# Kernel tuning notes

Hardware: AMD Instinct MI355X
Metric: run time of the kernel (lower is better)

## Reference

```python
import jax, jax.numpy as jnp
import numpy as np

N, E, D_IN, D_HID, D_OUT, R, B = 50000, 600000, 128, 128, 128, 8, 4


def setup_inputs() -> dict:
    key = jax.random.key(0)
    ks = jax.random.split(key, 12)
    s = 0.05
    return {
        "x": jax.random.normal(ks[0], (N, D_IN), jnp.float32),
        "edge_index": jax.random.randint(ks[1], (2, E), 0, N, jnp.int32),
        "edge_type": jax.random.randint(ks[2], (E,), 0, R, jnp.int32),
        "basis1": jax.random.normal(ks[3], (B, D_IN, D_HID), jnp.float32) * s,
        "comp1": jax.random.normal(ks[4], (R, B), jnp.float32) * s,
        "root1": jax.random.normal(ks[5], (D_IN, D_HID), jnp.float32) * s,
        "bias1": jnp.zeros((D_HID,), jnp.float32),
        "basis2": jax.random.normal(ks[6], (B, D_HID, D_OUT), jnp.float32) * s,
        "comp2": jax.random.normal(ks[7], (R, B), jnp.float32) * s,
        "root2": jax.random.normal(ks[8], (D_HID, D_OUT), jnp.float32) * s,
        "bias2": jnp.zeros((D_OUT,), jnp.float32),
    }


def _rgcn_conv(x, src, dst, etype, basis, comp, root, bias):
    # PyG RGCNConv (basis decomposition, aggr='mean' per relation):
    # out_i = x_i @ root + bias + sum_r mean_{e: type=r, dst=i} (x_src_e @ W_r)
    # W_r linear => aggregate raw features per (node, relation), then transform.
    n = x.shape[0]
    r = comp.shape[0]
    W = jnp.einsum('rb,bio->rio', comp, basis)          # [R, in, out]
    seg = dst * r + etype                               # [E] composite key
    agg = jax.ops.segment_sum(x[src], seg, num_segments=n * r)        # [N*R, in]
    cnt = jax.ops.segment_sum(jnp.ones_like(seg, x.dtype), seg, num_segments=n * r)
    mean = (agg / jnp.maximum(cnt, 1.0)[:, None]).reshape(n, r, -1)   # [N, R, in]
    return jnp.einsum('nri,rio->no', mean, W) + x @ root + bias


def reference(x, edge_index, edge_type, basis1, comp1, root1, bias1,
              basis2, comp2, root2, bias2):
    src, dst = edge_index[0], edge_index[1]
    h = _rgcn_conv(x, src, dst, edge_type, basis1, comp1, root1, bias1)
    h = jax.nn.relu(h)
    # dropout p=0.2 is identity in eval mode
    out = _rgcn_conv(h, src, dst, edge_type, basis2, comp2, root2, bias2)
    return out
```

## Files before the change

### kernel.cpp

```cpp
#include <hip/hip_runtime.h>

#define NN 50000
#define NE 600000
#define DD 128
#define RR 8
#define NBASIS 4
#define NR (NN * RR)
#define KTOT 640
#define KZ 512
#define MPAD 50048
#define KMASK 0x0FFFFFFF

typedef float f32x4 __attribute__((ext_vector_type(4)));
typedef float f32x2 __attribute__((ext_vector_type(2)));
typedef short bf16x8 __attribute__((ext_vector_type(8)));
typedef unsigned int u32x4 __attribute__((ext_vector_type(4)));

static __device__ __forceinline__ unsigned short f2b(float f) {
  union { float f; unsigned u; } c; c.f = f;
  unsigned u = c.u + 0x7fffu + ((c.u >> 16) & 1u);
  return (unsigned short)(u >> 16);
}
static __device__ __forceinline__ unsigned pack2(float lo, float hi) {
  return (unsigned)f2b(lo) | ((unsigned)f2b(hi) << 16);
}
static __device__ __forceinline__ float b2f_lo(unsigned v) {
  union { unsigned u; float f; } c; c.u = v << 16; return c.f;
}
static __device__ __forceinline__ float b2f_hi(unsigned v) {
  union { unsigned u; float f; } c; c.u = v & 0xffff0000u; return c.f;
}
static __device__ __forceinline__ f32x2 sp2(float s) {
  f32x2 r; r.x = s; r.y = s; return r;
}

static __device__ __forceinline__ void fma_bf(f32x2* A0, f32x2* A1, f32x2* A2,
                                              f32x2* A3, u32x4 v, float4 c) {
  f32x2 e0, e1, e2, e3;
  e0.x = b2f_lo(v.x); e0.y = b2f_hi(v.x);
  e1.x = b2f_lo(v.y); e1.y = b2f_hi(v.y);
  e2.x = b2f_lo(v.z); e2.y = b2f_hi(v.z);
  e3.x = b2f_lo(v.w); e3.y = b2f_hi(v.w);
  f32x2 cx = sp2(c.x), cy = sp2(c.y), cz = sp2(c.z), cw = sp2(c.w);
  A0[0] += cx * e0; A0[1] += cx * e1; A0[2] += cx * e2; A0[3] += cx * e3;
  A1[0] += cy * e0; A1[1] += cy * e1; A1[2] += cy * e2; A1[3] += cy * e3;
  A2[0] += cz * e0; A2[1] += cz * e1; A2[2] += cz * e2; A2[3] += cz * e3;
  A3[0] += cw * e0; A3[1] += cw * e1; A3[2] += cw * e2; A3[3] += cw * e3;
}

static __device__ __forceinline__ void reduce_store(
    const f32x2* A0, const f32x2* A1, const f32x2* A2, const f32x2* A3,
    int g, int q, int node, u32x4* __restrict__ Ab4) {
  float a0[8] = {A0[0].x, A0[0].y, A0[1].x, A0[1].y,
                 A0[2].x, A0[2].y, A0[3].x, A0[3].y};
  float a1[8] = {A1[0].x, A1[0].y, A1[1].x, A1[1].y,
                 A1[2].x, A1[2].y, A1[3].x, A1[3].y};
  float a2[8] = {A2[0].x, A2[0].y, A2[1].x, A2[1].y,
                 A2[2].x, A2[2].y, A2[3].x, A2[3].y};
  float a3[8] = {A3[0].x, A3[0].y, A3[1].x, A3[1].y,
                 A3[2].x, A3[2].y, A3[3].x, A3[3].y};
#pragma unroll
  for (int j = 0; j < 8; ++j) {
    a0[j] += __shfl_xor(a0[j], 16); a0[j] += __shfl_xor(a0[j], 32);
    a1[j] += __shfl_xor(a1[j], 16); a1[j] += __shfl_xor(a1[j], 32);
    a2[j] += __shfl_xor(a2[j], 16); a2[j] += __shfl_xor(a2[j], 32);
    a3[j] += __shfl_xor(a3[j], 16); a3[j] += __shfl_xor(a3[j], 32);
  }
  u32x4 wv;
  if (g == 0) {
    wv.x = pack2(a0[0], a0[1]); wv.y = pack2(a0[2], a0[3]);
    wv.z = pack2(a0[4], a0[5]); wv.w = pack2(a0[6], a0[7]);
  } else if (g == 1) {
    wv.x = pack2(a1[0], a1[1]); wv.y = pack2(a1[2], a1[3]);
    wv.z = pack2(a1[4], a1[5]); wv.w = pack2(a1[6], a1[7]);
  } else if (g == 2) {
    wv.x = pack2(a2[0], a2[1]); wv.y = pack2(a2[2], a2[3]);
    wv.z = pack2(a2[4], a2[5]); wv.w = pack2(a2[6], a2[7]);
  } else {
    wv.x = pack2(a3[0], a3[1]); wv.y = pack2(a3[2], a3[3]);
    wv.z = pack2(a3[4], a3[5]); wv.w = pack2(a3[6], a3[7]);
  }
  __builtin_nontemporal_store(wv, Ab4 + (size_t)node * 64 + g * 16 + q);
}

#define PREP_XB 12500
#define PREP_BT 320
#define PREP_CNT 2344
#define PREP_TOTAL (PREP_XB + 2 * PREP_BT + PREP_CNT)

__global__ __launch_bounds__(256) void prep_kernel(
    const float* __restrict__ x, const float* __restrict__ basis1,
    const float* __restrict__ root1, const float* __restrict__ basis2,
    const float* __restrict__ root2, const int* __restrict__ dst,
    const int* __restrict__ et, unsigned* __restrict__ xb,
    unsigned short* __restrict__ BT1, unsigned short* __restrict__ BT2,
    int* __restrict__ cnt) {
  int bid = blockIdx.x;
  int t = threadIdx.x;
  if (bid < PREP_XB) {
    int i = bid * 256 + t;
    float2 v = ((const float2*)x)[i];
    xb[i] = pack2(v.x, v.y);
  } else if (bid < PREP_XB + PREP_BT) {
    int idx = (bid - PREP_XB) * 256 + t;
    int c = idx / KTOT, k = idx - c * KTOT;
    float v = (k < 512) ? basis1[(size_t)((k >> 7) * DD + (k & 127)) * DD + c]
                        : root1[(size_t)(k - 512) * DD + c];
    BT1[idx] = f2b(v);
  } else if (bid < PREP_XB + 2 * PREP_BT) {
    int idx = (bid - PREP_XB - PREP_BT) * 256 + t;
    int c = idx / KTOT, k = idx - c * KTOT;
    float v = (k < 512) ? basis2[(size_t)((k >> 7) * DD + (k & 127)) * DD + c]
                        : root2[(size_t)(k - 512) * DD + c];
    BT2[idx] = f2b(v);
  } else {
    int e = (bid - PREP_XB - 2 * PREP_BT) * 256 + t;
    if (e < NE) atomicAdd(&cnt[dst[e] * RR + et[e]], 1);
  }
}

__global__ __launch_bounds__(256) void offs_kernel(
    const int* __restrict__ cnt, int2* __restrict__ od,
    int* __restrict__ curs, int* __restrict__ gcur) {
  __shared__ int s[256];
  __shared__ int base;
  int t = threadIdx.x;
  int i = blockIdx.x * 256 + t;
  int v = 0;
  if (i < NN) {
    const int4* c4 = (const int4*)cnt;
    int4 a = c4[i * 2];
    int4 b = c4[i * 2 + 1];
    v = a.x + a.y + a.z + a.w + b.x + b.y + b.z + b.w;
  }
  s[t] = v;
  __syncthreads();
  for (int off = 1; off < 256; off <<= 1) {
    int add = (t >= off) ? s[t - off] : 0;
    __syncthreads();
    s[t] += add;
    __syncthreads();
  }
  if (t == 255) base = atomicAdd(gcur, s[255]);
  __syncthreads();
  if (i < NN) {
    int o = base + s[t] - v;
    od[i] = make_int2(o, v);
    curs[i] = o;
  }
}

__global__ __launch_bounds__(256) void sort_kernel(
    const int* __restrict__ src, const int* __restrict__ dst,
    const int* __restrict__ et, int* __restrict__ curs,
    int* __restrict__ skey) {
  int e = blockIdx.x * 256 + threadIdx.x;
  if (e >= NE) return;
  int p = atomicAdd(&curs[dst[e]], 1);
  skey[p] = src[e] | (et[e] << 28);
}

__global__ __launch_bounds__(256) void agg_kernel(
    const u32x4* __restrict__ featb4,
    const int* __restrict__ skey, const int* __restrict__ cnt,
    const float* __restrict__ comp, const int2* __restrict__ od,
    u32x4* __restrict__ Ab4) {
  __shared__ float ccl[8][RR * NBASIS];
  int tid = threadIdx.x;
  int w = tid >> 6;
  int lane = tid & 63;
  int nA = blockIdx.x * 8 + w * 2;
  int nB = nA + 1;
  int g = lane >> 4;
  int q = lane & 15;

  {
    int which = lane >> 5;
    int idx = lane & 31;
    int node = nA + which;
    int c = cnt[node * RR + (idx >> 2)];
    ccl[w * 2 + which][idx] = comp[idx] * (1.0f / (float)max(c, 1));
  }
  __syncthreads();

  int2 odA = od[nA];
  int2 odB = od[nB];
  int begA = odA.x, dgA = odA.y;
  int begB = odB.x, dgB = odB.y;
  int lastA = min(begA + max(dgA, 1) - 1, NE - 1);
  int lastB = min(begB + max(dgB, 1) - 1, NE - 1);

  int pA0 = min(begA + g, lastA);
  int pA1 = min(begA + g + 4, lastA);
  int pA2 = min(begA + g + 8, lastA);
  int kA0 = skey[pA0], kA1 = skey[pA1], kA2 = skey[pA2];
  u32x4 vA0 = featb4[(size_t)(kA0 & KMASK) * 16 + q];
  u32x4 vA1 = featb4[(size_t)(kA1 & KMASK) * 16 + q];
  u32x4 vA2 = featb4[(size_t)(kA2 & KMASK) * 16 + q];

  int pB0 = min(begB + g, lastB);
  int pB1 = min(begB + g + 4, lastB);
  int pB2 = min(begB + g + 8, lastB);
  int kB0 = skey[pB0], kB1 = skey[pB1], kB2 = skey[pB2];
  u32x4 vB0 = featb4[(size_t)(kB0 & KMASK) * 16 + q];
  u32x4 vB1 = featb4[(size_t)(kB1 & KMASK) * 16 + q];
  u32x4 vB2 = featb4[(size_t)(kB2 & KMASK) * 16 + q];

  f32x2 A0[4] = {}, A1[4] = {}, A2[4] = {}, A3[4] = {};

  {
    const float4* cc4 = (const float4*)ccl[w * 2];
    float4 c0 = cc4[((unsigned)kA0) >> 28];
    float4 c1 = cc4[((unsigned)kA1) >> 28];
    float4 c2 = cc4[((unsigned)kA2) >> 28];
    float s0 = (g < dgA) ? 1.f : 0.f;
    float s1 = (g + 4 < dgA) ? 1.f : 0.f;
    float s2 = (g + 8 < dgA) ? 1.f : 0.f;
    c0.x *= s0; c0.y *= s0; c0.z *= s0; c0.w *= s0;
    c1.x *= s1; c1.y *= s1; c1.z *= s1; c1.w *= s1;
    c2.x *= s2; c2.y *= s2; c2.z *= s2; c2.w *= s2;
    fma_bf(A0, A1, A2, A3, vA0, c0);
    fma_bf(A0, A1, A2, A3, vA1, c1);
    fma_bf(A0, A1, A2, A3, vA2, c2);

    for (int i = g + 12; i < dgA; i += 12) {
      int p0 = begA + i;
      int p1 = min(p0 + 4, lastA);
      int p2 = min(p0 + 8, lastA);
      int k0 = skey[p0], k1 = skey[p1], k2 = skey[p2];
      u32x4 v0 = featb4[(size_t)(k0 & KMASK) * 16 + q];
      u32x4 v1 = featb4[(size_t)(k1 & KMASK) * 16 + q];
      u32x4 v2 = featb4[(size_t)(k2 & KMASK) * 16 + q];
      float4 c0t = cc4[((unsigned)k0) >> 28];
      float4 c1t = cc4[((unsigned)k1) >> 28];
      float4 c2t = cc4[((unsigned)k2) >> 28];
      float t1 = (i + 4 < dgA) ? 1.f : 0.f;
      float t2 = (i + 8 < dgA) ? 1.f : 0.f;
      c1t.x *= t1; c1t.y *= t1; c1t.z *= t1; c1t.w *= t1;
      c2t.x *= t2; c2t.y *= t2; c2t.z *= t2; c2t.w *= t2;
      fma_bf(A0, A1, A2, A3, v0, c0t);
      fma_bf(A0, A1, A2, A3, v1, c1t);
      fma_bf(A0, A1, A2, A3, v2, c2t);
    }
    reduce_store(A0, A1, A2, A3, g, q, nA, Ab4);
  }

  {
#pragma unroll
    for (int j = 0; j < 4; ++j) {
      A0[j] = sp2(0.f); A1[j] = sp2(0.f); A2[j] = sp2(0.f); A3[j] = sp2(0.f);
    }
    const float4* cc4 = (const float4*)ccl[w * 2 + 1];
    float4 c0 = cc4[((unsigned)kB0) >> 28];
    float4 c1 = cc4[((unsigned)kB1) >> 28];
    float4 c2 = cc4[((unsigned)kB2) >> 28];
    float s0 = (g < dgB) ? 1.f : 0.f;
    float s1 = (g + 4 < dgB) ? 1.f : 0.f;
    float s2 = (g + 8 < dgB) ? 1.f : 0.f;
    c0.x *= s0; c0.y *= s0; c0.z *= s0; c0.w *= s0;
    c1.x *= s1; c1.y *= s1; c1.z *= s1; c1.w *= s1;
    c2.x *= s2; c2.y *= s2; c2.z *= s2; c2.w *= s2;
    fma_bf(A0, A1, A2, A3, vB0, c0);
    fma_bf(A0, A1, A2, A3, vB1, c1);
    fma_bf(A0, A1, A2, A3, vB2, c2);

    for (int i = g + 12; i < dgB; i += 12) {
      int p0 = begB + i;
      int p1 = min(p0 + 4, lastB);
      int p2 = min(p0 + 8, lastB);
      int k0 = skey[p0], k1 = skey[p1], k2 = skey[p2];
      u32x4 v0 = featb4[(size_t)(k0 & KMASK) * 16 + q];
      u32x4 v1 = featb4[(size_t)(k1 & KMASK) * 16 + q];
      u32x4 v2 = featb4[(size_t)(k2 & KMASK) * 16 + q];
      float4 c0t = cc4[((unsigned)k0) >> 28];
      float4 c1t = cc4[((unsigned)k1) >> 28];
      float4 c2t = cc4[((unsigned)k2) >> 28];
      float t1 = (i + 4 < dgB) ? 1.f : 0.f;
      float t2 = (i + 8 < dgB) ? 1.f : 0.f;
      c1t.x *= t1; c1t.y *= t1; c1t.z *= t1; c1t.w *= t1;
      c2t.x *= t2; c2t.y *= t2; c2t.z *= t2; c2t.w *= t2;
      fma_bf(A0, A1, A2, A3, v0, c0t);
      fma_bf(A0, A1, A2, A3, v1, c1t);
      fma_bf(A0, A1, A2, A3, v2, c2t);
    }
    reduce_store(A0, A1, A2, A3, g, q, nB, Ab4);
  }
}

template <int OUT_BF16>
__global__ __launch_bounds__(256) void gemm_mfma(
    const unsigned short* __restrict__ Ab,
    const unsigned short* __restrict__ feat,
    const unsigned short* __restrict__ BT,
    const float* __restrict__ bias, void* __restrict__ Cout) {
  __shared__ unsigned short As[128][64];
  __shared__ unsigned short Bs[128][64];

  int tid = threadIdx.x;
  int row0 = blockIdx.x * 128;
  int lane = tid & 63;
  int wid = tid >> 6;
  int wr = (wid >> 1) * 64;
  int wc = (wid & 1) * 64;

  f32x4 acc[4][4] = {};

  for (int kt = 0; kt < KTOT; kt += 64) {
#pragma unroll
    for (int i = 0; i < 4; ++i) {
      int off = i * 256 + tid;
      int r = off >> 3;
      int ke = (off & 7) << 3;
      u32x4 av;
      if (kt < KZ)
        av = __builtin_nontemporal_load(
            (const u32x4*)(Ab + (size_t)(row0 + r) * KZ + kt + ke));
      else
        av = *(const u32x4*)(feat + (size_t)(row0 + r) * DD + (kt - KZ) + ke);
      *(u32x4*)((unsigned short*)As + (size_t)off * 8) = av;
      *(u32x4*)((unsigned short*)Bs + (size_t)off * 8) =
          *(const u32x4*)(BT + (size_t)r * KTOT + kt + ke);
    }
    __syncthreads();

#pragma unroll
    for (int kk = 0; kk < 2; ++kk) {
      int ko = kk * 32 + ((lane >> 4) << 3);
      bf16x8 a[4], b[4];
#pragma unroll
      for (int m = 0; m < 4; ++m)
        a[m] = *(const bf16x8*)&As[wr + m * 16 + (lane & 15)][ko];
#pragma unroll
      for (int n = 0; n < 4; ++n)
        b[n] = *(const bf16x8*)&Bs[wc + n * 16 + (lane & 15)][ko];
#pragma unroll
      for (int m = 0; m < 4; ++m)
#pragma unroll
        for (int n = 0; n < 4; ++n)
          acc[m][n] = __builtin_amdgcn_mfma_f32_16x16x32_bf16(
              a[m], b[n], acc[m][n], 0, 0, 0);
    }
    __syncthreads();
  }

#pragma unroll
  for (int n = 0; n < 4; ++n) {
    int col = wc + n * 16 + (lane & 15);
    float bb = bias[col];
#pragma unroll
    for (int m = 0; m < 4; ++m) {
      f32x4 v = acc[m][n];
#pragma unroll
      for (int j = 0; j < 4; ++j) {
        int row = row0 + wr + m * 16 + ((lane >> 4) << 2) + j;
        if (row < NN) {
          float o = v[j] + bb;
          if (OUT_BF16) {
            o = fmaxf(o, 0.f);
            ((unsigned short*)Cout)[(size_t)row * DD + col] = f2b(o);
          } else {
            ((float*)Cout)[(size_t)row * DD + col] = o;
          }
        }
      }
    }
  }
}

extern "C" void kernel_launch(void* const* d_in, const int* in_sizes, int n_in,
                              void* d_out, int out_size, void* d_ws,
                              size_t ws_size, hipStream_t stream) {
  const float* x      = (const float*)d_in[0];
  const int*   eidx   = (const int*)d_in[1];
  const int*   etype  = (const int*)d_in[2];
  const float* basis1 = (const float*)d_in[3];
  const float* comp1  = (const float*)d_in[4];
  const float* root1  = (const float*)d_in[5];
  const float* bias1  = (const float*)d_in[6];
  const float* basis2 = (const float*)d_in[7];
  const float* comp2  = (const float*)d_in[8];
  const float* root2  = (const float*)d_in[9];
  const float* bias2  = (const float*)d_in[10];
  float* out = (float*)d_out;

  const int* src = eidx;
  const int* dst = eidx + NE;

  unsigned short* Ab  = (unsigned short*)d_ws;
  unsigned short* xb  = Ab + (size_t)MPAD * KZ;
  unsigned short* hb  = xb + (size_t)MPAD * DD;
  unsigned short* BT1 = hb + (size_t)MPAD * DD;
  unsigned short* BT2 = BT1 + (size_t)DD * KTOT;
  int*  skey = (int*)(BT2 + (size_t)DD * KTOT);
  int*  cnt  = skey + NE;
  int*  gcur = cnt + NR;
  int2* od   = (int2*)(gcur + 4);
  int*  curs = (int*)(od + NN);

  const int NB = (NN + 255) / 256;
  const int EB = (NE + 255) / 256;

  hipMemsetAsync(cnt, 0, (size_t)(NR + 4) * sizeof(int), stream);
  prep_kernel<<<PREP_TOTAL, 256, 0, stream>>>(
      x, basis1, root1, basis2, root2, dst, etype, (unsigned*)xb, BT1, BT2,
      cnt);
  offs_kernel<<<NB, 256, 0, stream>>>(cnt, od, curs, gcur);
  sort_kernel<<<EB, 256, 0, stream>>>(src, dst, etype, curs, skey);

  int agg_blocks = NN / 8;
  int gemm_blocks = MPAD / 128;

  agg_kernel<<<agg_blocks, 256, 0, stream>>>((const u32x4*)xb, skey, cnt,
                                             comp1, od, (u32x4*)Ab);
  gemm_mfma<1><<<gemm_blocks, 256, 0, stream>>>(Ab, xb, BT1, bias1, hb);
  agg_kernel<<<agg_blocks, 256, 0, stream>>>((const u32x4*)hb, skey, cnt,
                                             comp2, od, (u32x4*)Ab);
  gemm_mfma<0><<<gemm_blocks, 256, 0, stream>>>(Ab, hb, BT2, bias2, out);
}
```

Measured before the change: 234.1 us.

## Fuse neighbor aggregation with MFMA GEMM through LDS per 32-node tile

```diff
diff --git a/kernel.cpp b/kernel.cpp
--- a/kernel.cpp
+++ b/kernel.cpp
@@ -10,6 +10,7 @@
 #define KZ 512
 #define MPAD 50048
 #define KMASK 0x0FFFFFFF
+#define NPB 32
 
 typedef float f32x4 __attribute__((ext_vector_type(4)));
 typedef float f32x2 __attribute__((ext_vector_type(2)));
@@ -48,9 +49,9 @@
   A3[0] += cw * e0; A3[1] += cw * e1; A3[2] += cw * e2; A3[3] += cw * e3;
 }
 
-static __device__ __forceinline__ void reduce_store(
+static __device__ __forceinline__ void reduce_store_lds(
     const f32x2* A0, const f32x2* A1, const f32x2* A2, const f32x2* A3,
-    int g, int q, int node, u32x4* __restrict__ Ab4) {
+    int g, int q, unsigned short* zp ) {
   float a0[8] = {A0[0].x, A0[0].y, A0[1].x, A0[1].y,
                  A0[2].x, A0[2].y, A0[3].x, A0[3].y};
   float a1[8] = {A1[0].x, A1[0].y, A1[1].x, A1[1].y,
@@ -80,7 +81,7 @@
     wv.x = pack2(a3[0], a3[1]); wv.y = pack2(a3[2], a3[3]);
     wv.z = pack2(a3[4], a3[5]); wv.w = pack2(a3[6], a3[7]);
   }
-  __builtin_nontemporal_store(wv, Ab4 + (size_t)node * 64 + g * 16 + q);
+  *(u32x4*)(zp + g * 128 + q * 8) = wv;
 }
 
 #define PREP_XB 12500
@@ -160,150 +161,142 @@
   skey[p] = src[e] | (et[e] << 28);
 }
 
-__global__ __launch_bounds__(256) void agg_kernel(
+template <int OUT_BF16>
+__global__ __launch_bounds__(256) void rgcn_fused(
     const u32x4* __restrict__ featb4,
+    const unsigned short* __restrict__ feat,
     const int* __restrict__ skey, const int* __restrict__ cnt,
     const float* __restrict__ comp, const int2* __restrict__ od,
-    u32x4* __restrict__ Ab4) {
+    const unsigned short* __restrict__ BT,
+    const float* __restrict__ bias, void* __restrict__ Cout) {
+  __shared__ unsigned short zA[NPB][520];
+  __shared__ unsigned short Bs[128][72];
+  __shared__ unsigned short fS[NPB][72];
   __shared__ float ccl[8][RR * NBASIS];
+
   int tid = threadIdx.x;
   int w = tid >> 6;
   int lane = tid & 63;
-  int nA = blockIdx.x * 8 + w * 2;
-  int nB = nA + 1;
   int g = lane >> 4;
   int q = lane & 15;
-
-  {
-    int which = lane >> 5;
-    int idx = lane & 31;
-    int node = nA + which;
-    int c = cnt[node * RR + (idx >> 2)];
-    ccl[w * 2 + which][idx] = comp[idx] * (1.0f / (float)max(c, 1));
-  }
-  __syncthreads();
-
-  int2 odA = od[nA];
-  int2 odB = od[nB];
-  int begA = odA.x, dgA = odA.y;
-  int begB = odB.x, dgB = odB.y;
-  int lastA = min(begA + max(dgA, 1) - 1, NE - 1);
-  int lastB = min(begB + max(dgB, 1) - 1, NE - 1);
-
-  int pA0 = min(begA + g, lastA);
-  int pA1 = min(begA + g + 4, lastA);
-  int pA2 = min(begA + g + 8, lastA);
-  int kA0 = skey[pA0], kA1 = skey[pA1], kA2 = skey[pA2];
-  u32x4 vA0 = featb4[(size_t)(kA0 & KMASK) * 16 + q];
-  u32x4 vA1 = featb4[(size_t)(kA1 & KMASK) * 16 + q];
-  u32x4 vA2 = featb4[(size_t)(kA2 & KMASK) * 16 + q];
-
-  int pB0 = min(begB + g, lastB);
-  int pB1 = min(begB + g + 4, lastB);
-  int pB2 = min(begB + g + 8, lastB);
-  int kB0 = skey[pB0], kB1 = skey[pB1], kB2 = skey[pB2];
-  u32x4 vB0 = featb4[(size_t)(kB0 & KMASK) * 16 + q];
-  u32x4 vB1 = featb4[(size_t)(kB1 & KMASK) * 16 + q];
-  u32x4 vB2 = featb4[(size_t)(kB2 & KMASK) * 16 + q];
-
-  f32x2 A0[4] = {}, A1[4] = {}, A2[4] = {}, A3[4] = {};
-
-  {
-    const float4* cc4 = (const float4*)ccl[w * 2];
-    float4 c0 = cc4[((unsigned)kA0) >> 28];
-    float4 c1 = cc4[((unsigned)kA1) >> 28];
-    float4 c2 = cc4[((unsigned)kA2) >> 28];
-    float s0 = (g < dgA) ? 1.f : 0.f;
-    float s1 = (g + 4 < dgA) ? 1.f : 0.f;
-    float s2 = (g + 8 < dgA) ? 1.f : 0.f;
-    c0.x *= s0; c0.y *= s0; c0.z *= s0; c0.w *= s0;
-    c1.x *= s1; c1.y *= s1; c1.z *= s1; c1.w *= s1;
-    c2.x *= s2; c2.y *= s2; c2.z *= s2; c2.w *= s2;
-    fma_bf(A0, A1, A2, A3, vA0, c0);
-    fma_bf(A0, A1, A2, A3, vA1, c1);
-    fma_bf(A0, A1, A2, A3, vA2, c2);
-
-    for (int i = g + 12; i < dgA; i += 12) {
-      int p0 = begA + i;
-      int p1 = min(p0 + 4, lastA);
-      int p2 = min(p0 + 8, lastA);
-      int k0 = skey[p0], k1 = skey[p1], k2 = skey[p2];
-      u32x4 v0 = featb4[(size_t)(k0 & KMASK) * 16 + q];
-      u32x4 v1 = featb4[(size_t)(k1 & KMASK) * 16 + q];
-      u32x4 v2 = featb4[(size_t)(k2 & KMASK) * 16 + q];
-      float4 c0t = cc4[((unsigned)k0) >> 28];
-      float4 c1t = cc4[((unsigned)k1) >> 28];
-      float4 c2t = cc4[((unsigned)k2) >> 28];
-      float t1 = (i + 4 < dgA) ? 1.f : 0.f;
-      float t2 = (i + 8 < dgA) ? 1.f : 0.f;
-      c1t.x *= t1; c1t.y *= t1; c1t.z *= t1; c1t.w *= t1;
-      c2t.x *= t2; c2t.y *= t2; c2t.z *= t2; c2t.w *= t2;
-      fma_bf(A0, A1, A2, A3, v0, c0t);
-      fma_bf(A0, A1, A2, A3, v1, c1t);
-      fma_bf(A0, A1, A2, A3, v2, c2t);
-    }
-    reduce_store(A0, A1, A2, A3, g, q, nA, Ab4);
-  }
-
-  {
-#pragma unroll
-    for (int j = 0; j < 4; ++j) {
-      A0[j] = sp2(0.f); A1[j] = sp2(0.f); A2[j] = sp2(0.f); A3[j] = sp2(0.f);
-    }
-    const float4* cc4 = (const float4*)ccl[w * 2 + 1];
-    float4 c0 = cc4[((unsigned)kB0) >> 28];
-    float4 c1 = cc4[((unsigned)kB1) >> 28];
-    float4 c2 = cc4[((unsigned)kB2) >> 28];
-    float s0 = (g < dgB) ? 1.f : 0.f;
-    float s1 = (g + 4 < dgB) ? 1.f : 0.f;
-    float s2 = (g + 8 < dgB) ? 1.f : 0.f;
-    c0.x *= s0; c0.y *= s0; c0.z *= s0; c0.w *= s0;
-    c1.x *= s1; c1.y *= s1; c1.z *= s1; c1.w *= s1;
-    c2.x *= s2; c2.y *= s2; c2.z *= s2; c2.w *= s2;
-    fma_bf(A0, A1, A2, A3, vB0, c0);
-    fma_bf(A0, A1, A2, A3, vB1, c1);
-    fma_bf(A0, A1, A2, A3, vB2, c2);
-
-    for (int i = g + 12; i < dgB; i += 12) {
-      int p0 = begB + i;
-      int p1 = min(p0 + 4, lastB);
-      int p2 = min(p0 + 8, lastB);
-      int k0 = skey[p0], k1 = skey[p1], k2 = skey[p2];
-      u32x4 v0 = featb4[(size_t)(k0 & KMASK) * 16 + q];
-      u32x4 v1 = featb4[(size_t)(k1 & KMASK) * 16 + q];
-      u32x4 v2 = featb4[(size_t)(k2 & KMASK) * 16 + q];
-      float4 c0t = cc4[((unsigned)k0) >> 28];
-      float4 c1t = cc4[((unsigned)k1) >> 28];
-      float4 c2t = cc4[((unsigned)k2) >> 28];
-      float t1 = (i + 4 < dgB) ? 1.f : 0.f;
-      float t2 = (i + 8 < dgB) ? 1.f : 0.f;
-      c1t.x *= t1; c1t.y *= t1; c1t.z *= t1; c1t.w *= t1;
-      c2t.x *= t2; c2t.y *= t2; c2t.z *= t2; c2t.w *= t2;
-      fma_bf(A0, A1, A2, A3, v0, c0t);
-      fma_bf(A0, A1, A2, A3, v1, c1t);
-      fma_bf(A0, A1, A2, A3, v2, c2t);
-    }
-    reduce_store(A0, A1, A2, A3, g, q, nB, Ab4);
-  }
-}
-
-template <int OUT_BF16>
-__global__ __launch_bounds__(256) void gemm_mfma(
-    const unsigned short* __restrict__ Ab,
-    const unsigned short* __restrict__ feat,
-    const unsigned short* __restrict__ BT,
-    const float* __restrict__ bias, void* __restrict__ Cout) {
-  __shared__ unsigned short As[128][64];
-  __shared__ unsigned short Bs[128][64];
-
-  int tid = threadIdx.x;
-  int row0 = blockIdx.x * 128;
-  int lane = tid & 63;
-  int wid = tid >> 6;
-  int wr = (wid >> 1) * 64;
-  int wc = (wid & 1) * 64;
-
-  f32x4 acc[4][4] = {};
+  int nb = blockIdx.x * NPB;
+
+  for (int rr = 0; rr < 4; ++rr) {
+    int nA = nb + w * 8 + rr * 2;
+    int nB = nA + 1;
+    int ncA = min(nA, NN - 1);
+    int ncB = min(nB, NN - 1);
+    {
+      int which = lane >> 5;
+      int idx = lane & 31;
+      int nodec = which ? ncB : ncA;
+      int c = cnt[nodec * RR + (idx >> 2)];
+      ccl[w * 2 + which][idx] = comp[idx] * (1.0f / (float)max(c, 1));
+    }
+    int2 odA = od[ncA];
+    int2 odB = od[ncB];
+    int begA = odA.x, dgA = (nA < NN) ? odA.y : 0;
+    int begB = odB.x, dgB = (nB < NN) ? odB.y : 0;
+    int lastA = min(begA + max(dgA, 1) - 1, NE - 1);
+    int lastB = min(begB + max(dgB, 1) - 1, NE - 1);
+
+    int pA0 = min(begA + g, lastA);
+    int pA1 = min(begA + g + 4, lastA);
+    int pA2 = min(begA + g + 8, lastA);
+    int kA0 = skey[pA0], kA1 = skey[pA1], kA2 = skey[pA2];
+    u32x4 vA0 = featb4[(size_t)(kA0 & KMASK) * 16 + q];
+    u32x4 vA1 = featb4[(size_t)(kA1 & KMASK) * 16 + q];
+    u32x4 vA2 = featb4[(size_t)(kA2 & KMASK) * 16 + q];
+
+    int pB0 = min(begB + g, lastB);
+    int pB1 = min(begB + g + 4, lastB);
+    int pB2 = min(begB + g + 8, lastB);
+    int kB0 = skey[pB0], kB1 = skey[pB1], kB2 = skey[pB2];
+    u32x4 vB0 = featb4[(size_t)(kB0 & KMASK) * 16 + q];
+    u32x4 vB1 = featb4[(size_t)(kB1 & KMASK) * 16 + q];
+    u32x4 vB2 = featb4[(size_t)(kB2 & KMASK) * 16 + q];
+
+    f32x2 A0[4] = {}, A1[4] = {}, A2[4] = {}, A3[4] = {};
+
+    {
+      const float4* cc4 = (const float4*)ccl[w * 2];
+      float4 c0 = cc4[((unsigned)kA0) >> 28];
+      float4 c1 = cc4[((unsigned)kA1) >> 28];
+      float4 c2 = cc4[((unsigned)kA2) >> 28];
+      float s0 = (g < dgA) ? 1.f : 0.f;
+      float s1 = (g + 4 < dgA) ? 1.f : 0.f;
+      float s2 = (g + 8 < dgA) ? 1.f : 0.f;
+      c0.x *= s0; c0.y *= s0; c0.z *= s0; c0.w *= s0;
+      c1.x *= s1; c1.y *= s1; c1.z *= s1; c1.w *= s1;
+      c2.x *= s2; c2.y *= s2; c2.z *= s2; c2.w *= s2;
+      fma_bf(A0, A1, A2, A3, vA0, c0);
+      fma_bf(A0, A1, A2, A3, vA1, c1);
+      fma_bf(A0, A1, A2, A3, vA2, c2);
+      for (int i = g + 12; i < dgA; i += 12) {
+        int p0 = begA + i;
+        int p1 = min(p0 + 4, lastA);
+        int p2 = min(p0 + 8, lastA);
+        int k0 = skey[p0], k1 = skey[p1], k2 = skey[p2];
+        u32x4 v0 = featb4[(size_t)(k0 & KMASK) * 16 + q];
+        u32x4 v1 = featb4[(size_t)(k1 & KMASK) * 16 + q];
+        u32x4 v2 = featb4[(size_t)(k2 & KMASK) * 16 + q];
+        float4 c0t = cc4[((unsigned)k0) >> 28];
+        float4 c1t = cc4[((unsigned)k1) >> 28];
+        float4 c2t = cc4[((unsigned)k2) >> 28];
+        float t1 = (i + 4 < dgA) ? 1.f : 0.f;
+        float t2 = (i + 8 < dgA) ? 1.f : 0.f;
+        c1t.x *= t1; c1t.y *= t1; c1t.z *= t1; c1t.w *= t1;
+        c2t.x *= t2; c2t.y *= t2; c2t.z *= t2; c2t.w *= t2;
+        fma_bf(A0, A1, A2, A3, v0, c0t);
+        fma_bf(A0, A1, A2, A3, v1, c1t);
+        fma_bf(A0, A1, A2, A3, v2, c2t);
+      }
+      reduce_store_lds(A0, A1, A2, A3, g, q, &zA[w * 8 + rr * 2][0]);
+    }
+
+    {
+#pragma unroll
+      for (int j = 0; j < 4; ++j) {
+        A0[j] = sp2(0.f); A1[j] = sp2(0.f); A2[j] = sp2(0.f); A3[j] = sp2(0.f);
+      }
+      const float4* cc4 = (const float4*)ccl[w * 2 + 1];
+      float4 c0 = cc4[((unsigned)kB0) >> 28];
+      float4 c1 = cc4[((unsigned)kB1) >> 28];
+      float4 c2 = cc4[((unsigned)kB2) >> 28];
+      float s0 = (g < dgB) ? 1.f : 0.f;
+      float s1 = (g + 4 < dgB) ? 1.f : 0.f;
+      float s2 = (g + 8 < dgB) ? 1.f : 0.f;
+      c0.x *= s0; c0.y *= s0; c0.z *= s0; c0.w *= s0;
+      c1.x *= s1; c1.y *= s1; c1.z *= s1; c1.w *= s1;
+      c2.x *= s2; c2.y *= s2; c2.z *= s2; c2.w *= s2;
+      fma_bf(A0, A1, A2, A3, vB0, c0);
+      fma_bf(A0, A1, A2, A3, vB1, c1);
+      fma_bf(A0, A1, A2, A3, vB2, c2);
+      for (int i = g + 12; i < dgB; i += 12) {
+        int p0 = begB + i;
+        int p1 = min(p0 + 4, lastB);
+        int p2 = min(p0 + 8, lastB);
+        int k0 = skey[p0], k1 = skey[p1], k2 = skey[p2];
+        u32x4 v0 = featb4[(size_t)(k0 & KMASK) * 16 + q];
+        u32x4 v1 = featb4[(size_t)(k1 & KMASK) * 16 + q];
+        u32x4 v2 = featb4[(size_t)(k2 & KMASK) * 16 + q];
+        float4 c0t = cc4[((unsigned)k0) >> 28];
+        float4 c1t = cc4[((unsigned)k1) >> 28];
+        float4 c2t = cc4[((unsigned)k2) >> 28];
+        float t1 = (i + 4 < dgB) ? 1.f : 0.f;
+        float t2 = (i + 8 < dgB) ? 1.f : 0.f;
+        c1t.x *= t1; c1t.y *= t1; c1t.z *= t1; c1t.w *= t1;
+        c2t.x *= t2; c2t.y *= t2; c2t.z *= t2; c2t.w *= t2;
+        fma_bf(A0, A1, A2, A3, v0, c0t);
+        fma_bf(A0, A1, A2, A3, v1, c1t);
+        fma_bf(A0, A1, A2, A3, v2, c2t);
+      }
+      reduce_store_lds(A0, A1, A2, A3, g, q, &zA[w * 8 + rr * 2 + 1][0]);
+    }
+  }
+
+  int wc = w * 32;
+  f32x4 acc[2][2] = {};
 
   for (int kt = 0; kt < KTOT; kt += 64) {
 #pragma unroll
@@ -311,32 +304,32 @@
       int off = i * 256 + tid;
       int r = off >> 3;
       int ke = (off & 7) << 3;
-      u32x4 av;
-      if (kt < KZ)
-        av = __builtin_nontemporal_load(
-            (const u32x4*)(Ab + (size_t)(row0 + r) * KZ + kt + ke));
-      else
-        av = *(const u32x4*)(feat + (size_t)(row0 + r) * DD + (kt - KZ) + ke);
-      *(u32x4*)((unsigned short*)As + (size_t)off * 8) = av;
-      *(u32x4*)((unsigned short*)Bs + (size_t)off * 8) =
-          *(const u32x4*)(BT + (size_t)r * KTOT + kt + ke);
+      *(u32x4*)&Bs[r][ke] = *(const u32x4*)(BT + (size_t)r * KTOT + kt + ke);
+    }
+    if (kt >= KZ) {
+      int r = tid >> 3;
+      int ke = (tid & 7) << 3;
+      *(u32x4*)&fS[r][ke] =
+          *(const u32x4*)(feat + (size_t)(nb + r) * DD + (kt - KZ) + ke);
     }
     __syncthreads();
 
 #pragma unroll
     for (int kk = 0; kk < 2; ++kk) {
       int ko = kk * 32 + ((lane >> 4) << 3);
-      bf16x8 a[4], b[4];
-#pragma unroll
-      for (int m = 0; m < 4; ++m)
-        a[m] = *(const bf16x8*)&As[wr + m * 16 + (lane & 15)][ko];
-#pragma unroll
-      for (int n = 0; n < 4; ++n)
+      bf16x8 a[2], b[2];
+#pragma unroll
+      for (int m = 0; m < 2; ++m)
+        a[m] = (kt < KZ)
+                   ? *(const bf16x8*)&zA[m * 16 + (lane & 15)][kt + ko]
+                   : *(const bf16x8*)&fS[m * 16 + (lane & 15)][ko];
+#pragma unroll
+      for (int n = 0; n < 2; ++n)
         b[n] = *(const bf16x8*)&Bs[wc + n * 16 + (lane & 15)][ko];
 #pragma unroll
-      for (int m = 0; m < 4; ++m)
-#pragma unroll
-        for (int n = 0; n < 4; ++n)
+      for (int m = 0; m < 2; ++m)
+#pragma unroll
+        for (int n = 0; n < 2; ++n)
           acc[m][n] = __builtin_amdgcn_mfma_f32_16x16x32_bf16(
               a[m], b[n], acc[m][n], 0, 0, 0);
     }
@@ -344,15 +337,15 @@
   }
 
 #pragma unroll
-  for (int n = 0; n < 4; ++n) {
+  for (int n = 0; n < 2; ++n) {
     int col = wc + n * 16 + (lane & 15);
     float bb = bias[col];
 #pragma unroll
-    for (int m = 0; m < 4; ++m) {
+    for (int m = 0; m < 2; ++m) {
       f32x4 v = acc[m][n];
 #pragma unroll
       for (int j = 0; j < 4; ++j) {
-        int row = row0 + wr + m * 16 + ((lane >> 4) << 2) + j;
+        int row = nb + m * 16 + ((lane >> 4) << 2) + j;
         if (row < NN) {
           float o = v[j] + bb;
           if (OUT_BF16) {
@@ -386,8 +379,7 @@
   const int* src = eidx;
   const int* dst = eidx + NE;
 
-  unsigned short* Ab  = (unsigned short*)d_ws;
-  unsigned short* xb  = Ab + (size_t)MPAD * KZ;
+  unsigned short* xb  = (unsigned short*)d_ws;
   unsigned short* hb  = xb + (size_t)MPAD * DD;
   unsigned short* BT1 = hb + (size_t)MPAD * DD;
   unsigned short* BT2 = BT1 + (size_t)DD * KTOT;
@@ -407,13 +399,10 @@
   offs_kernel<<<NB, 256, 0, stream>>>(cnt, od, curs, gcur);
   sort_kernel<<<EB, 256, 0, stream>>>(src, dst, etype, curs, skey);
 
-  int agg_blocks = NN / 8;
-  int gemm_blocks = MPAD / 128;
-
-  agg_kernel<<<agg_blocks, 256, 0, stream>>>((const u32x4*)xb, skey, cnt,
-                                             comp1, od, (u32x4*)Ab);
-  gemm_mfma<1><<<gemm_blocks, 256, 0, stream>>>(Ab, xb, BT1, bias1, hb);
-  agg_kernel<<<agg_blocks, 256, 0, stream>>>((const u32x4*)hb, skey, cnt,
-                                             comp2, od, (u32x4*)Ab);
-  gemm_mfma<0><<<gemm_blocks, 256, 0, stream>>>(Ab, hb, BT2, bias2, out);
-}
+  int fused_blocks = (NN + NPB - 1) / NPB;
+
+  rgcn_fused<1><<<fused_blocks, 256, 0, stream>>>(
+      (const u32x4*)xb, xb, skey, cnt, comp1, od, BT1, bias1, hb);
+  rgcn_fused<0><<<fused_blocks, 256, 0, stream>>>(
+      (const u32x4*)hb, hb, skey, cnt, comp2, od, BT2, bias2, out);
+}
```

After: 258.7 us. 10.5% more time.
